# Performance work log

Hardware: AMD Instinct MI355X
Metric: run time of the kernel (lower is better)

The kernel has to match this reference:

```python
import jax, jax.numpy as jnp
import numpy as np

# QMon (monDEQ, Winston & Kolter): conv pre-net -> MONSingleConv + MONBorderReLU solved
# with Peaceman-Rachford splitting -> border crop -> MLP head.
BATCH = 256
C = 64            # DEQ channels
N = 9             # DEQ spatial dim (in_dim=9)
K = 3             # MONSingleConv kernel size
M_STRONG = 0.1    # m (strong monotonicity)
ALPHA = 1.0
TOL = 1e-5
MAX_ITER = 50
OUT_FEATURES = 18


def conv2d(x, w, b=None, stride=1):
    y = jax.lax.conv_general_dilated(x, w, (stride, stride), 'VALID',
                                     dimension_numbers=('NCHW', 'OIHW', 'NCHW'))
    if b is not None:
        y = y + b[None, :, None, None]
    return y


def circ_conv(x, w, b=None):
    # circular-padded 'same' conv (cpad + valid conv in the torch code)
    p = (w.shape[2] - 1) // 2
    xp = jnp.pad(x, ((0, 0), (0, 0), (p, p), (p, p)), mode='wrap')
    return conv2d(xp, w, b)


def circ_conv_T(x, w):
    # adjoint of circular conv = circular conv with spatially-flipped, channel-transposed kernel
    wt = jnp.transpose(jnp.flip(w, (2, 3)), (1, 0, 2, 3))
    return circ_conv(x, wt)


def W_multiply(z, A_w, g):
    # W z = (1-m) z - g * A^T A z, with A Frobenius-normalized
    An = A_w / jnp.linalg.norm(A_w)
    Az = circ_conv(z, An)
    ATAz = circ_conv_T(Az, An)
    return (1.0 - M_STRONG) * z - g * ATAz


def build_inverse(A_w, g, n):
    # ((1+alpha) I - alpha W)^{-1} per 2D-DFT frequency (circular conv is block-circulant)
    An = A_w / jnp.linalg.norm(A_w)
    co, ci, k, _ = An.shape
    p = (k - 1) // 2
    kimg = jnp.zeros((co, ci, n, n), An.dtype)
    for dx in range(k):
        for dy in range(k):
            kimg = kimg.at[:, :, (dx - p) % n, (dy - p) % n].set(An[:, :, dx, dy])
    Af = jnp.conj(jnp.fft.fft2(kimg)).transpose(2, 3, 0, 1)  # (n,n,O,I): A_hat(w)
    I = jnp.eye(co, dtype=Af.dtype)
    c = (1.0 + ALPHA) - ALPHA * (1.0 - M_STRONG)
    Mmat = c * I + (ALPHA * g).astype(Af.dtype) * jnp.einsum('xyoi,xyoj->xyij', jnp.conj(Af), Af)
    return jnp.linalg.inv(Mmat)  # (n,n,C,C) complex


def apply_inverse(Vinv, z):
    zf = jnp.fft.fft2(z)                                  # (B,C,n,n)
    yf = jnp.einsum('xyoc,bcxy->boxy', Vinv, zf)
    return jnp.real(jnp.fft.ifft2(yf)).astype(z.dtype)


def mon_deq(xpre, U_w, U_b, A_w, g):
    n = xpre.shape[-1]
    bias = circ_conv(xpre, U_w, U_b)
    Vinv = build_inverse(A_w, g, n)
    mask = jnp.pad(jnp.ones((n - 2, n - 2), xpre.dtype), 1)[None, None]  # MONBorderReLU border=1
    brelu = lambda v: jax.nn.relu(v) * mask
    z0 = jnp.zeros_like(bias)

    def body(state):
        z, u, err, it = state
        u12 = 2.0 * z - u
        z12 = apply_inverse(Vinv, u12 + ALPHA * bias)
        un = 2.0 * z12 - u12
        zn = brelu(un)
        err = jnp.linalg.norm(zn - z) / (1e-6 + jnp.linalg.norm(zn))
        return zn, un, err, it + 1

    def cond(state):
        _, _, err, it = state
        return (err > TOL) & (it < MAX_ITER)

    z, u, err, it = jax.lax.while_loop(cond, body, (z0, z0, jnp.asarray(1.0, xpre.dtype), 0))
    # final pass with the linear operator (as in the torch forward after the no_grad solve)
    return brelu(W_multiply(z, A_w, g) + bias)


def setup_inputs() -> dict:
    key = jax.random.key(0)
    ks = jax.random.split(key, 12)

    def u(k, shape, fan_in):
        b = 1.0 / np.sqrt(fan_in)
        return jax.random.uniform(k, shape, jnp.float32, -b, b)

    x = jax.random.uniform(ks[0], (BATCH, 4, 84, 84), jnp.float32) * 255.0
    return dict(
        x=x,
        conv1_w=u(ks[1], (32, 4, 8, 8), 4 * 8 * 8), conv1_b=u(ks[2], (32,), 4 * 8 * 8),
        conv2_w=u(ks[3], (64, 32, 4, 4), 32 * 4 * 4), conv2_b=u(ks[4], (64,), 32 * 4 * 4),
        U_w=u(ks[5], (C, C, K, K), C * K * K), U_b=u(ks[6], (C,), C * K * K),
        A_w=u(ks[7], (C, C, K, K), C * K * K), g=jnp.asarray(1.0, jnp.float32),
        fc1_w=u(ks[8], (512, 3136), 3136), fc1_b=u(ks[9], (512,), 3136),
        fc2_w=u(ks[10], (OUT_FEATURES, 512), 512), fc2_b=u(ks[11], (OUT_FEATURES,), 512),
    )


def reference(x, conv1_w, conv1_b, conv2_w, conv2_b, U_w, U_b, A_w, g,
              fc1_w, fc1_b, fc2_w, fc2_b):
    h = jax.nn.relu(conv2d(x / 255.0, conv1_w, conv1_b, stride=4))   # (B,32,20,20)
    h = jax.nn.relu(conv2d(h, conv2_w, conv2_b, stride=2))           # (B,64,9,9)
    z = mon_deq(h, U_w, U_b, A_w, g)                                 # (B,64,9,9)
    z = z[:, :, 1:-1, 1:-1].reshape(z.shape[0], -1)                  # (B,3136)
    h = jax.nn.relu(z @ fc1_w.T + fc1_b)
    return h @ fc2_w.T + fc2_b
```

## Files before the change

### kernel.cpp

```cpp
#include <hip/hip_runtime.h>


#define NB 256
#define NCH 64
#define NP 81
#define NIMG (NB*NCH)
#define MAXIT 50
#define NCAN 41
#define CANON(l) ((l) < 5 ? (l) : (l) + 4)

constexpr float C9[9] = {
  1.0f, 0.76604444311897803f, 0.17364817766693041f, -0.5f,
  -0.93969262078590843f, -0.93969262078590843f, -0.5f,
  0.17364817766693041f, 0.76604444311897803f };
constexpr float S9[9] = {
  0.0f, 0.64278760968653936f, 0.98480775301220802f, 0.86602540378443871f,
  0.34202014332566877f, -0.34202014332566877f, -0.86602540378443871f,
  -0.98480775301220802f, -0.64278760968653936f };

__constant__ float COS9[9] = {
  1.0f, 0.76604444311897803f, 0.17364817766693041f, -0.5f,
  -0.93969262078590843f, -0.93969262078590843f, -0.5f,
  0.17364817766693041f, 0.76604444311897803f };
__constant__ float SIN9[9] = {
  0.0f, 0.64278760968653936f, 0.98480775301220802f, 0.86602540378443871f,
  0.34202014332566877f, -0.34202014332566877f, -0.86602540378443871f,
  -0.98480775301220802f, -0.64278760968653936f };

__global__ __launch_bounds__(256) void k_norm(const float* __restrict__ Aw,
                                              float* __restrict__ sc) {
    __shared__ float red[256];
    float s = 0.f;
    for (int i = threadIdx.x; i < 64*64*9; i += 256) { float a = Aw[i]; s += a*a; }
    red[threadIdx.x] = s; __syncthreads();
    for (int w = 128; w > 0; w >>= 1) {
        if (threadIdx.x < w) red[threadIdx.x] += red[threadIdx.x + w];
        __syncthreads();
    }
    if (threadIdx.x == 0) { float n = sqrtf(red[0]); sc[0] = n; sc[1] = 1.f/n; }
}

__global__ __launch_bounds__(512, 4) void k_conv1(const float* __restrict__ x,
                                                  const float* __restrict__ w,
                                                  const float* __restrict__ bb,
                                                  float* __restrict__ y) {
    __shared__ float xl[2*7056];
    int blk = blockIdx.x, tid = threadIdx.x;
    int b = blk >> 1, og = (blk & 1) << 4;
    float acc[16];
    #pragma unroll
    for (int o = 0; o < 16; ++o) acc[o] = 0.f;
    int p = tid, oy = p/20, ox = p%20;
    for (int cp = 0; cp < 2; ++cp) {
        __syncthreads();
        const float4* xg = (const float4*)(x + b*28224 + cp*14112);
        for (int i = tid; i < 3528; i += 512) ((float4*)xl)[i] = xg[i];
        __syncthreads();
        if (p < 400) {
            #pragma unroll
            for (int ci = 0; ci < 2; ++ci)
            #pragma unroll
            for (int ky = 0; ky < 8; ++ky) {
                const float* xr = xl + ci*7056 + (oy*4+ky)*84 + ox*4;
                float4 x0 = *(const float4*)xr;
                float4 x1 = *(const float4*)(xr+4);
                const float* wr = w + og*256 + (cp*2+ci)*64 + ky*8;
                #pragma unroll
                for (int o = 0; o < 16; ++o) {
                    const float* wo = wr + o*256;
                    acc[o] += x0.x*wo[0] + x0.y*wo[1] + x0.z*wo[2] + x0.w*wo[3]
                            + x1.x*wo[4] + x1.y*wo[5] + x1.z*wo[6] + x1.w*wo[7];
                }
            }
        }
    }
    if (p < 400) {
        #pragma unroll
        for (int o = 0; o < 16; ++o)
            y[b*12800 + (og+o)*400 + p] = fmaxf(acc[o]*(1.f/255.f) + bb[og+o], 0.f);
    }
}

__global__ __launch_bounds__(512, 4) void k_conv2(const float* __restrict__ h1,
                                                  const float* __restrict__ w2,
                                                  const float* __restrict__ b2,
                                                  float* __restrict__ h2) {
    int blk = blockIdx.x, tid = threadIdx.x;
    int b = blk >> 1, og = (blk & 1) << 5;
    __shared__ float hl[12800];
    for (int i = tid; i < 12800; i += 512) {
        int ci = i / 400, pix = i % 400, iy = pix / 20, ix = pix % 20;
        hl[ci*400 + ((iy&1)*2 + (ix&1))*100 + (iy>>1)*10 + (ix>>1)] = h1[b*12800 + i];
    }
    __syncthreads();
    for (int idx = tid; idx < 2592; idx += 512) {
        int o = og + idx/81, p = idx%81, oy = p/9, ox = p%9;
        float acc = 0.f;
        const float* wo = w2 + o*512;
        for (int ci = 0; ci < 32; ci++) {
            const float* base = hl + ci*400;
            const float* wb = wo + ci*16;
            #pragma unroll
            for (int ky = 0; ky < 4; ky++)
            #pragma unroll
            for (int kx = 0; kx < 4; kx++)
                acc += base[((ky&1)*2 + (kx&1))*100 + (oy + (ky>>1))*10 + (ox + (kx>>1))]
                     * wb[ky*4 + kx];
        }
        h2[b*5184 + o*81 + p] = fmaxf(acc + b2[o], 0.f);
    }
}

__global__ __launch_bounds__(512, 4) void k_bias(const float* __restrict__ h2,
                                                 const float* __restrict__ Uw,
                                                 const float* __restrict__ Ub,
                                                 float* __restrict__ biasT) {
    int blk = blockIdx.x, tid = threadIdx.x;
    int b = blk >> 1, og = (blk & 1) << 5;
    __shared__ float h2l[5184];
    __shared__ float bt[2592];
    for (int i = tid; i < 5184; i += 512) h2l[i] = h2[b*5184 + i];
    __syncthreads();
    for (int idx = tid; idx < 2592; idx += 512) {
        int oc = idx/81, o = og + oc, p = idx%81, i0 = p/9, j0 = p%9;
        int im = (i0+8)%9, ip = (i0+1)%9, jm = (j0+8)%9, jp = (j0+1)%9;
        int r0 = im*9, r1 = i0*9, r2 = ip*9;
        float acc = 0.f;
        const float* wo = Uw + o*576;
        for (int ci = 0; ci < 64; ci++) {
            const float* hb = h2l + ci*81;
            const float* wb = wo + ci*9;
            acc += hb[r0+jm]*wb[0] + hb[r0+j0]*wb[1] + hb[r0+jp]*wb[2]
                 + hb[r1+jm]*wb[3] + hb[r1+j0]*wb[4] + hb[r1+jp]*wb[5]
                 + hb[r2+jm]*wb[6] + hb[r2+j0]*wb[7] + hb[r2+jp]*wb[8];
        }
        bt[oc*81 + p] = acc + Ub[o];
    }
    __syncthreads();
    for (int idx = tid; idx < 2592; idx += 512) {
        int p = idx >> 5, o32 = idx & 31;
        biasT[p*NIMG + b*64 + og + o32] = bt[o32*81 + p];
    }
}

__global__ __launch_bounds__(256) void k_af(const float* __restrict__ Aw,
                                            const float* __restrict__ sc,
                                            float2* __restrict__ Af) {
    int l = blockIdx.x; int f = CANON(l);
    int x = f/9, y = f%9;
    float inv = sc[1];
    for (int pr = threadIdx.x; pr < 4096; pr += 256) {
        const float* a = Aw + pr*9;
        float re = 0.f, im = 0.f;
        #pragma unroll
        for (int dx = 0; dx < 3; dx++)
        #pragma unroll
        for (int dy = 0; dy < 3; dy++) {
            int tt = (x*(dx+8) + y*(dy+8)) % 9;
            float v = a[dx*3+dy] * inv;
            re += v * COS9[tt]; im += v * SIN9[tt];
        }
        Af[f*4096 + pr] = make_float2(re, im);
    }
}

__global__ __launch_bounds__(256) void k_mw(const float2* __restrict__ Af,
                                            const float* __restrict__ gp,
                                            float2* __restrict__ Mmat,
                                            float2* __restrict__ WmT) {
    int l = blockIdx.x; int f = CANON(l);
    float g = gp[0];
    __shared__ float2 Al[4096];
    for (int i = threadIdx.x; i < 4096; i += 256) Al[i] = Af[f*4096 + i];
    __syncthreads();
    for (int e = threadIdx.x; e < 4096; e += 256) {
        int i = e >> 6, j = e & 63;
        float sr = 0.f, si = 0.f;
        for (int o = 0; o < 64; o++) {
            float2 a = Al[o*64 + i], b = Al[o*64 + j];
            sr += a.x*b.x + a.y*b.y;
            si += a.x*b.y - a.y*b.x;
        }
        Mmat[f*4096 + e] = make_float2((i==j ? 1.1f : 0.f) + g*sr, g*si);
        WmT [f*4096 + j*64 + i] = make_float2((i==j ? 0.9f : 0.f) - g*sr, -g*si);
    }
}

__global__ __launch_bounds__(64) void k_inv(float2* __restrict__ Mio) {
    int f = CANON((int)blockIdx.x);
    __shared__ float2 M[64*65];
    int j = threadIdx.x;
    float2* Mg = Mio + f*4096;
    for (int i = 0; i < 64; ++i) M[i*65 + j] = Mg[i*64 + j];
    __builtin_amdgcn_wave_barrier();
    for (int k = 0; k < 64; ++k) {
        float2 d = M[k*65 + k];
        float den = 1.f / (d.x*d.x + d.y*d.y);
        float pr = d.x*den, pi = -d.y*den;
        float2 mk = M[k*65 + j];
        float2 rkj = (j == k) ? make_float2(pr, pi)
                              : make_float2(mk.x*pr - mk.y*pi, mk.x*pi + mk.y*pr);
        __builtin_amdgcn_wave_barrier();
        #pragma unroll 4
        for (int i = 0; i < 64; ++i) {
            float2 fi  = M[i*65 + k];
            float2 cur = M[i*65 + j];
            float2 nv;
            if (i == k)      nv = rkj;
            else if (j == k) nv = make_float2(-(fi.x*pr - fi.y*pi),
                                              -(fi.x*pi + fi.y*pr));
            else             nv = make_float2(cur.x - (fi.x*rkj.x - fi.y*rkj.y),
                                              cur.y - (fi.x*rkj.y + fi.y*rkj.x));
            __builtin_amdgcn_wave_barrier();
            M[i*65 + j] = nv;
            __builtin_amdgcn_wave_barrier();
        }
    }
    for (int c = 0; c < 64; ++c) Mg[c*64 + j] = M[j*65 + c];
}

__global__ __launch_bounds__(576) void k_fft(const float* __restrict__ biasT,
                                             float2* __restrict__ Tf) {
    __shared__ float2 T1[81*64];
    int lane = threadIdx.x & 63, j = threadIdx.x >> 6;
    int gimg = blockIdx.x*64 + lane;
    {
        int r = j;
        float tn[9];
        #pragma unroll
        for (int xc = 0; xc < 9; ++xc) tn[xc] = biasT[(r*9 + xc)*NIMG + gimg];
        #pragma unroll
        for (int ky = 0; ky < 9; ++ky) {
            float sr = 0.f, si = 0.f;
            #pragma unroll
            for (int xx = 0; xx < 9; ++xx) {
                const int m = (ky*xx) % 9;
                sr += tn[xx]*C9[m];
                si -= tn[xx]*S9[m];
            }
            T1[(r*9 + ky)*64 + lane] = make_float2(sr, si);
        }
    }
    __syncthreads();
    {
        int ky = j;
        float2 s[9];
        #pragma unroll
        for (int r = 0; r < 9; ++r) s[r] = T1[(r*9 + ky)*64 + lane];
        #pragma unroll
        for (int kx = 0; kx < 5; ++kx) {
            float fr = 0.f, fi = 0.f;
            #pragma unroll
            for (int r = 0; r < 9; ++r) {
                const int m = (kx*r) % 9;
                fr += s[r].x*C9[m] + s[r].y*S9[m];
                fi += s[r].y*C9[m] - s[r].x*S9[m];
            }
            if (kx > 0 || ky < 5)
                Tf[(kx*9 + ky)*NIMG + gimg] = make_float2(fr, fi);
        }
    }
}

__global__ __launch_bounds__(256) void k_mv(const float2* __restrict__ Tf,
                                            float2* __restrict__ Yf,
                                            const float2* __restrict__ V) {
    int l = blockIdx.x >> 4, bc = blockIdx.x & 15;
    int f = CANON(l);
    int lane = threadIdx.x & 63;
    int wid  = __builtin_amdgcn_readfirstlane((int)(threadIdx.x >> 6));
    int b0 = bc*16 + wid*4;
    const float2* Vg = V + f*4096 + lane;
    const float2* Tg = Tf + f*NIMG + b0*64;
    float2 a0 = make_float2(0.f,0.f), a1 = a0, a2 = a0, a3 = a0;
    #pragma unroll 8
    for (int c = 0; c < 64; ++c) {
        float2 v = Vg[c*64];
        float2 t0 = Tg[c], t1 = Tg[64+c], t2 = Tg[128+c], t3 = Tg[192+c];
        a0.x += v.x*t0.x - v.y*t0.y; a0.y += v.x*t0.y + v.y*t0.x;
        a1.x += v.x*t1.x - v.y*t1.y; a1.y += v.x*t1.y + v.y*t1.x;
        a2.x += v.x*t2.x - v.y*t2.y; a2.y += v.x*t2.y + v.y*t2.x;
        a3.x += v.x*t3.x - v.y*t3.y; a3.y += v.x*t3.y + v.y*t3.x;
    }
    float2* Yg = Yf + f*NIMG + b0*64 + lane;
    Yg[0] = a0; Yg[64] = a1; Yg[128] = a2; Yg[192] = a3;
}

__global__ __launch_bounds__(576) void k_fuse(const float2* __restrict__ Yf,
                                              float* __restrict__ u12T,
                                              const float* __restrict__ biasT,
                                              float2* __restrict__ Tf,
                                              int last) {
    __shared__ float2 T1[81*64];
    int lane = threadIdx.x & 63, j = threadIdx.x >> 6;
    int gimg = blockIdx.x*64 + lane;
    {
        int ky = j;
        float2 y[9];
        #pragma unroll
        for (int kx = 0; kx < 9; ++kx) {
            int fc; bool cj;
            if (kx == 0)      { cj = (ky >= 5); fc = cj ? (9 - ky) : ky; }
            else if (kx <= 4) { cj = false;     fc = kx*9 + ky; }
            else              { cj = true;      fc = (9-kx)*9 + (ky ? 9-ky : 0); }
            float2 a = Yf[fc*NIMG + gimg];
            y[kx] = make_float2(a.x, cj ? -a.y : a.y);
        }
        #pragma unroll
        for (int r = 0; r < 9; ++r) {
            float sr = 0.f, si = 0.f;
            #pragma unroll
            for (int kx = 0; kx < 9; ++kx) {
                const int m = (r*kx) % 9;
                sr += y[kx].x*C9[m] - y[kx].y*S9[m];
                si += y[kx].x*S9[m] + y[kx].y*C9[m];
            }
            T1[(r*9 + ky)*64 + lane] = make_float2(sr, si);
        }
    }
    __syncthreads();
    {
        int r = j;
        float2 t1[9];
        #pragma unroll
        for (int ky = 0; ky < 9; ++ky) t1[ky] = T1[(r*9 + ky)*64 + lane];
        float tn[9];
        #pragma unroll
        for (int xc = 0; xc < 9; ++xc) {
            float yr = 0.f;
            #pragma unroll
            for (int ky = 0; ky < 9; ++ky) {
                const int m = (xc*ky) % 9;
                yr += t1[ky].x*C9[m] - t1[ky].y*S9[m];
            }
            yr *= (1.f/81.f);
            int gi = (r*9 + xc)*NIMG + gimg;
            float u12v = u12T[gi];
            float un = 2.f*yr - u12v;
            bool interior = (r >= 1 && r <= 7 && xc >= 1 && xc <= 7);
            float zn = interior ? fmaxf(un, 0.f) : 0.f;
            float u12n = 2.f*zn - un;
            u12T[gi] = u12n;
            tn[xc] = last ? zn : (u12n + biasT[gi]);
        }
        #pragma unroll
        for (int ky = 0; ky < 9; ++ky) {
            float sr = 0.f, si = 0.f;
            #pragma unroll
            for (int xx = 0; xx < 9; ++xx) {
                const int m = (ky*xx) % 9;
                sr += tn[xx]*C9[m];
                si -= tn[xx]*S9[m];
            }
            T1[(r*9 + ky)*64 + lane] = make_float2(sr, si);
        }
    }
    __syncthreads();
    {
        int ky = j;
        float2 s[9];
        #pragma unroll
        for (int r = 0; r < 9; ++r) s[r] = T1[(r*9 + ky)*64 + lane];
        #pragma unroll
        for (int kx = 0; kx < 5; ++kx) {
            float fr = 0.f, fi = 0.f;
            #pragma unroll
            for (int r = 0; r < 9; ++r) {
                const int m = (kx*r) % 9;
                fr += s[r].x*C9[m] + s[r].y*S9[m];
                fi += s[r].y*C9[m] - s[r].x*S9[m];
            }
            if (kx > 0 || ky < 5)
                Tf[(kx*9 + ky)*NIMG + gimg] = make_float2(fr, fi);
        }
    }
}

__global__ __launch_bounds__(576) void k_crop(const float2* __restrict__ Yf,
                                              const float* __restrict__ biasT,
                                              float* __restrict__ zc) {
    __shared__ float2 T1[81*64];
    int lane = threadIdx.x & 63, j = threadIdx.x >> 6;
    int gimg = blockIdx.x*64 + lane;
    {
        int ky = j;
        float2 y[9];
        #pragma unroll
        for (int kx = 0; kx < 9; ++kx) {
            int fc; bool cj;
            if (kx == 0)      { cj = (ky >= 5); fc = cj ? (9 - ky) : ky; }
            else if (kx <= 4) { cj = false;     fc = kx*9 + ky; }
            else              { cj = true;      fc = (9-kx)*9 + (ky ? 9-ky : 0); }
            float2 a = Yf[fc*NIMG + gimg];
            y[kx] = make_float2(a.x, cj ? -a.y : a.y);
        }
        #pragma unroll
        for (int r = 0; r < 9; ++r) {
            float sr = 0.f, si = 0.f;
            #pragma unroll
            for (int kx = 0; kx < 9; ++kx) {
                const int m = (r*kx) % 9;
                sr += y[kx].x*C9[m] - y[kx].y*S9[m];
                si += y[kx].x*S9[m] + y[kx].y*C9[m];
            }
            T1[(r*9 + ky)*64 + lane] = make_float2(sr, si);
        }
    }
    __syncthreads();
    if (j >= 1 && j <= 7) {
        int r = j;
        float2 t1[9];
        #pragma unroll
        for (int ky = 0; ky < 9; ++ky) t1[ky] = T1[(r*9 + ky)*64 + lane];
        float* zr = zc + (gimg >> 6)*3136 + (gimg & 63)*49 + (r-1)*7;
        #pragma unroll
        for (int xc = 1; xc < 8; ++xc) {
            float yr = 0.f;
            #pragma unroll
            for (int ky = 0; ky < 9; ++ky) {
                const int m = (xc*ky) % 9;
                yr += t1[ky].x*C9[m] - t1[ky].y*S9[m];
            }
            yr *= (1.f/81.f);
            zr[xc-1] = fmaxf(yr + biasT[(r*9 + xc)*NIMG + gimg], 0.f);
        }
    }
}

__global__ __launch_bounds__(256) void k_fc1(const float* __restrict__ A,
                                             const float* __restrict__ W,
                                             const float* __restrict__ bb,
                                             float* __restrict__ H) {
    int bt = blockIdx.x >> 5, ot = blockIdx.x & 31;
    int b0 = bt*16, o0 = ot*16;
    __shared__ float At[16][65], Bt[16][65];
    int tid = threadIdx.x;
    int row = tid >> 6, col = tid & 63;
    int tb = tid >> 4, to = tid & 15;
    float acc = 0.f;
    for (int k0 = 0; k0 < 3136; k0 += 64) {
        #pragma unroll
        for (int s = 0; s < 4; s++) {
            int rr = row + s*4;
            At[rr][col] = A[(b0+rr)*3136 + k0 + col];
            Bt[rr][col] = W[(o0+rr)*3136 + k0 + col];
        }
        __syncthreads();
        #pragma unroll
        for (int kk = 0; kk < 64; kk++)
            acc += At[tb][kk] * Bt[to][kk];
        __syncthreads();
    }
    H[(b0+tb)*512 + o0+to] = fmaxf(acc + bb[o0+to], 0.f);
}

__global__ __launch_bounds__(256) void k_fc2(const float* __restrict__ H,
                                             const float* __restrict__ W,
                                             const float* __restrict__ bb,
                                             float* __restrict__ out) {
    int idx = blockIdx.x*256 + threadIdx.x;
    if (idx >= 4608) return;
    int b = idx/18, o = idx%18;
    const float* h = H + b*512;
    const float* w = W + o*512;
    float acc = 0.f;
    for (int k = 0; k < 512; k++) acc += h[k]*w[k];
    out[idx] = acc + bb[o];
}

extern "C" void kernel_launch(void* const* d_in, const int* in_sizes, int n_in,
                              void* d_out, int out_size, void* d_ws, size_t ws_size,
                              hipStream_t stream) {
    (void)in_sizes; (void)n_in; (void)out_size; (void)ws_size;
    const float* x   = (const float*)d_in[0];
    const float* c1w = (const float*)d_in[1];
    const float* c1b = (const float*)d_in[2];
    const float* c2w = (const float*)d_in[3];
    const float* c2b = (const float*)d_in[4];
    const float* Uw  = (const float*)d_in[5];
    const float* Ub  = (const float*)d_in[6];
    const float* Aw  = (const float*)d_in[7];
    const float* gp  = (const float*)d_in[8];
    const float* f1w = (const float*)d_in[9];
    const float* f1b = (const float*)d_in[10];
    const float* f2w = (const float*)d_in[11];
    const float* f2b = (const float*)d_in[12];

    float* ws = (float*)d_ws;
    float*  h1    = ws + 0;
    float2* Tf    = (float2*)(ws + 0);
    float*  biasT = ws + 3276800;
    float*  u12T  = ws + 4603904;
    float2* Yf    = (float2*)(ws + 5931008);
    float2* Af    = (float2*)(ws + 8585216);
    float2* Minv  = (float2*)(ws + 9248768);
    float2* WmT   = (float2*)(ws + 9912320);
    float*  zc    = ws + 10575872;
    float*  hfc   = ws + 11378688;
    float*  sc    = ws + 11509760;
    float*  h2    = ws + 11509764;

    hipMemsetAsync(u12T, 0, (size_t)1327104*sizeof(float), stream);

    k_norm <<<1,   256, 0, stream>>>(Aw, sc);
    k_conv1<<<512, 512, 0, stream>>>(x, c1w, c1b, h1);
    k_conv2<<<512, 512, 0, stream>>>(h1, c2w, c2b, h2);
    k_bias <<<512, 512, 0, stream>>>(h2, Uw, Ub, biasT);
    k_af   <<<NCAN,256, 0, stream>>>(Aw, sc, Af);
    k_mw   <<<NCAN,256, 0, stream>>>(Af, gp, Minv, WmT);
    k_inv  <<<NCAN,64,  0, stream>>>(Minv);

    k_fft<<<256, 576, 0, stream>>>(biasT, Tf);
    for (int it = 0; it < MAXIT; it++) {
        k_mv  <<<NCAN*16, 256, 0, stream>>>(Tf, Yf, Minv);
        k_fuse<<<256,     576, 0, stream>>>(Yf, u12T, biasT, Tf, it == MAXIT-1);
    }
    k_mv  <<<NCAN*16, 256, 0, stream>>>(Tf, Yf, WmT);
    k_crop<<<256,     576, 0, stream>>>(Yf, biasT, zc);

    k_fc1<<<512, 256, 0, stream>>>(zc, f1w, f1b, hfc);
    k_fc2<<<18,  256, 0, stream>>>(hfc, f2w, f2b, (float*)d_out);
}
```

Measured before the change: 2.086 ms.

## Parallelize matrix inversion across 256 threads and split k_mw over four blocks

The Gauss-Jordan inversion of each 64x64 complex matrix now runs with 256 threads instead of one wavefront. Each thread keeps 16 entries of a row in registers, and the pivot row and column are broadcast through double-buffered shared arrays with block barriers. The k_mw Gram-matrix kernel is split into four blocks per frequency so more CUs work on it. These are one-time setup kernels outside the 50-iteration loop, so they can only affect a small part of total time. The change adds block-wide syncs per pivot step.

Result: faster. 1.977 ms (-5.2%).

```diff
diff --git a/kernel.cpp b/kernel.cpp
--- a/kernel.cpp
+++ b/kernel.cpp
@@ -168,12 +168,15 @@
                                             const float* __restrict__ gp,
                                             float2* __restrict__ Mmat,
                                             float2* __restrict__ WmT) {
-    int l = blockIdx.x; int f = CANON(l);
+    int l = blockIdx.x >> 2, q = blockIdx.x & 3;
+    int f = CANON(l);
     float g = gp[0];
     __shared__ float2 Al[4096];
     for (int i = threadIdx.x; i < 4096; i += 256) Al[i] = Af[f*4096 + i];
     __syncthreads();
-    for (int e = threadIdx.x; e < 4096; e += 256) {
+    int e = q*1024 + threadIdx.x;
+    #pragma unroll
+    for (int rep = 0; rep < 4; ++rep, e += 256) {
         int i = e >> 6, j = e & 63;
         float sr = 0.f, si = 0.f;
         for (int o = 0; o < 64; o++) {
@@ -186,37 +189,55 @@
     }
 }
 
-__global__ __launch_bounds__(64) void k_inv(float2* __restrict__ Mio) {
+__global__ __launch_bounds__(256) void k_inv(float2* __restrict__ Mio) {
     int f = CANON((int)blockIdx.x);
-    __shared__ float2 M[64*65];
-    int j = threadIdx.x;
+    __shared__ float2 Mt[64*65];
+    __shared__ float2 rowk[2][64];
+    __shared__ float2 fcol[2][64];
+    int tid = threadIdx.x;
+    int i = tid & 63, jg = tid >> 6;
     float2* Mg = Mio + f*4096;
-    for (int i = 0; i < 64; ++i) M[i*65 + j] = Mg[i*64 + j];
-    __builtin_amdgcn_wave_barrier();
+    for (int e = tid; e < 4096; e += 256) Mt[(e>>6)*65 + (e&63)] = Mg[e];
+    __syncthreads();
+    float2 r[16];
+    #pragma unroll
+    for (int jj = 0; jj < 16; ++jj) r[jj] = Mt[i*65 + jg*16 + jj];
+
     for (int k = 0; k < 64; ++k) {
-        float2 d = M[k*65 + k];
+        int buf = k & 1;
+        if (i == k) {
+            #pragma unroll
+            for (int jj = 0; jj < 16; ++jj) rowk[buf][jg*16 + jj] = r[jj];
+        }
+        if (jg == (k >> 4)) fcol[buf][i] = r[k & 15];
+        __syncthreads();
+        float2 d = rowk[buf][k];
         float den = 1.f / (d.x*d.x + d.y*d.y);
         float pr = d.x*den, pi = -d.y*den;
-        float2 mk = M[k*65 + j];
-        float2 rkj = (j == k) ? make_float2(pr, pi)
-                              : make_float2(mk.x*pr - mk.y*pi, mk.x*pi + mk.y*pr);
-        __builtin_amdgcn_wave_barrier();
-        #pragma unroll 4
-        for (int i = 0; i < 64; ++i) {
-            float2 fi  = M[i*65 + k];
-            float2 cur = M[i*65 + j];
-            float2 nv;
-            if (i == k)      nv = rkj;
-            else if (j == k) nv = make_float2(-(fi.x*pr - fi.y*pi),
-                                              -(fi.x*pi + fi.y*pr));
-            else             nv = make_float2(cur.x - (fi.x*rkj.x - fi.y*rkj.y),
-                                              cur.y - (fi.x*rkj.y + fi.y*rkj.x));
-            __builtin_amdgcn_wave_barrier();
-            M[i*65 + j] = nv;
-            __builtin_amdgcn_wave_barrier();
-        }
-    }
-    for (int c = 0; c < 64; ++c) Mg[c*64 + j] = M[j*65 + c];
+        float2 fi = fcol[buf][i];
+        bool piv = (i == k);
+        #pragma unroll
+        for (int jj = 0; jj < 16; ++jj) {
+            int j = jg*16 + jj;
+            float2 rw = rowk[buf][j];
+            float2 rkj = (j == k) ? make_float2(pr, pi)
+                                  : make_float2(rw.x*pr - rw.y*pi,
+                                                rw.x*pi + rw.y*pr);
+            if (piv) {
+                r[jj] = rkj;
+            } else {
+                float bx = (j == k) ? 0.f : r[jj].x;
+                float by = (j == k) ? 0.f : r[jj].y;
+                r[jj] = make_float2(bx - (fi.x*rkj.x - fi.y*rkj.y),
+                                    by - (fi.x*rkj.y + fi.y*rkj.x));
+            }
+        }
+    }
+    __syncthreads();
+    #pragma unroll
+    for (int jj = 0; jj < 16; ++jj) Mt[(jg*16 + jj)*65 + i] = r[jj];
+    __syncthreads();
+    for (int e = tid; e < 4096; e += 256) Mg[e] = Mt[(e>>6)*65 + (e&63)];
 }
 
 __global__ __launch_bounds__(576) void k_fft(const float* __restrict__ biasT,
@@ -502,13 +523,13 @@
 
     hipMemsetAsync(u12T, 0, (size_t)1327104*sizeof(float), stream);
 
-    k_norm <<<1,   256, 0, stream>>>(Aw, sc);
-    k_conv1<<<512, 512, 0, stream>>>(x, c1w, c1b, h1);
-    k_conv2<<<512, 512, 0, stream>>>(h1, c2w, c2b, h2);
-    k_bias <<<512, 512, 0, stream>>>(h2, Uw, Ub, biasT);
-    k_af   <<<NCAN,256, 0, stream>>>(Aw, sc, Af);
-    k_mw   <<<NCAN,256, 0, stream>>>(Af, gp, Minv, WmT);
-    k_inv  <<<NCAN,64,  0, stream>>>(Minv);
+    k_norm <<<1,     256, 0, stream>>>(Aw, sc);
+    k_conv1<<<512,   512, 0, stream>>>(x, c1w, c1b, h1);
+    k_conv2<<<512,   512, 0, stream>>>(h1, c2w, c2b, h2);
+    k_bias <<<512,   512, 0, stream>>>(h2, Uw, Ub, biasT);
+    k_af   <<<NCAN,  256, 0, stream>>>(Aw, sc, Af);
+    k_mw   <<<NCAN*4,256, 0, stream>>>(Af, gp, Minv, WmT);
+    k_inv  <<<NCAN,  256, 0, stream>>>(Minv);
 
     k_fft<<<256, 576, 0, stream>>>(biasT, Tf);
     for (int it = 0; it < MAXIT; it++) {
```
